# Optimization experiments

Measured on AMD Instinct MI355X. Metric: run time of the kernel, lower is better.

## Reference

```python
import jax, jax.numpy as jnp
import numpy as np

B, QUE, VAL, D = 4, 128, 128, 512

def setup_inputs() -> dict:
    key = jax.random.key(0)
    k = jax.random.split(key, 8)
    return {
        "qs_1": jax.random.normal(k[0], (B, QUE, D), jnp.float32),
        "qs_2": jax.random.normal(k[1], (B, QUE, D), jnp.float32),  # unused by forward, kept for signature fidelity
        "ks":   jax.random.normal(k[2], (B, VAL, D), jnp.float32),
        "vs":   jax.random.normal(k[3], (B, VAL, D), jnp.float32),
        "sg_mask": jax.random.randint(k[4], (B, VAL), 0, 2).astype(bool),  # True = masked
        "W1":  jax.random.normal(k[5], (D, D), jnp.float32) / np.sqrt(D),
        "b1":  jnp.zeros((D,), jnp.float32),
        "Wse": jax.random.normal(k[6], (D, D), jnp.float32) / np.sqrt(D),
        "bse": jnp.zeros((D,), jnp.float32),
        "W2":  jax.random.normal(k[7], (D, 1), jnp.float32) / np.sqrt(D),
        "b2":  jnp.zeros((1,), jnp.float32),
    }

def reference(qs_1, qs_2, ks, vs, sg_mask, W1, b1, Wse, bse, W2, b2):
    # Pairwise query-key elementwise product: [B, que, val, d]
    x = qs_1[:, :, None, :] * ks[:, None, :, :]
    # linear1: Linear(d,d) + ReLU (dropout = identity at eval)
    h = jax.nn.relu(jnp.einsum('bqvd,de->bqve', x, W1) + b1)
    # linear2: Linear(d,1) + ReLU -> scalar score per (q, v) pair
    s = jax.nn.relu(jnp.einsum('bqvd,do->bqvo', h, W2) + b2)[..., 0]  # [B, que, val]
    m = sg_mask[:, None, :]                      # [B, 1, val], True = masked out
    # masked mean of h over the val axis (masked_fill(0) then divide by valid count)
    h = jnp.where(m[..., None], 0.0, h)
    denom = jnp.sum(~sg_mask, axis=-1).astype(h.dtype)      # [B]
    mean = h.sum(axis=2) / denom[:, None, None]             # [B, que, d]
    # squeeze-excitation gate: sigmoid(relu(Linear(d,d)))
    gate = jax.nn.sigmoid(jax.nn.relu(mean @ Wse + bse))    # [B, que, d]
    # masked softmax over val, weighted sum of values
    s = jnp.where(m, -1e9, s)
    w = jax.nn.softmax(s, axis=-1)                          # [B, que, val]
    out = jnp.einsum('bqv,bvd->bqd', w, vs)                 # [B, que, d]
    return gate * out
```

## Files before the change

kernel.cpp:

```cpp
#include <hip/hip_runtime.h>
#include <stdint.h>
#include <stddef.h>

#define BDIM 4
#define QUE  128
#define VAL  128
#define DD   512
#define BQ   (BDIM*QUE)
#define BK   64

typedef float    f32x4 __attribute__((ext_vector_type(4)));
typedef float    f32x2 __attribute__((ext_vector_type(2)));
typedef _Float16 f16x8 __attribute__((ext_vector_type(8)));
typedef _Float16 f16x4 __attribute__((ext_vector_type(4)));
typedef _Float16 f16x2 __attribute__((ext_vector_type(2)));

typedef const __attribute__((address_space(1))) void* gas_ptr;
typedef __attribute__((address_space(3))) void*       las_ptr;

__device__ __forceinline__ void async_copy16(const void* g, void* l) {
    __builtin_amdgcn_global_load_lds((gas_ptr)g, (las_ptr)l, 16, 0, 0);
}

__global__ __launch_bounds__(256) void prep_kernel(const float* __restrict__ W1,
                                                   _Float16* __restrict__ W1T,
                                                   const float* __restrict__ Wse,
                                                   _Float16* __restrict__ WseT,
                                                   const float* __restrict__ vs,
                                                   _Float16* __restrict__ vsT,
                                                   const float* __restrict__ qs1,
                                                   _Float16* __restrict__ qH,
                                                   const float* __restrict__ ks,
                                                   _Float16* __restrict__ ksH) {
    const int gx = blockIdx.x, gy = blockIdx.y;
    if (gy >= 36) {
        const float* src = (gy == 36) ? qs1 : ks;
        _Float16*    dst = (gy == 36) ? qH  : ksH;
        size_t base = (size_t)gx * 16384 + threadIdx.x * 4;
        #pragma unroll 4
        for (int i = 0; i < 16; ++i) {
            f32x4 w = *(const f32x4*)(src + base + (size_t)i * 1024);
            f16x4 h;
            h[0] = (_Float16)w[0]; h[1] = (_Float16)w[1];
            h[2] = (_Float16)w[2]; h[3] = (_Float16)w[3];
            *(f16x4*)(dst + base + (size_t)i * 1024) = h;
        }
        return;
    }
    __shared__ float tile[32][33];
    const int tx = threadIdx.x & 31;
    const int ty = threadIdx.x >> 5;
    if (gy < 32) {
        const float* src = (gy < 16) ? W1  : Wse;
        _Float16*    dst = (gy < 16) ? W1T : WseT;
        int a0 = gx * 32;
        int b0 = (gy & 15) * 32;
        #pragma unroll
        for (int r = 0; r < 4; ++r)
            tile[ty + r*8][tx] = src[(size_t)(a0 + ty + r*8) * DD + b0 + tx];
        __syncthreads();
        #pragma unroll
        for (int r = 0; r < 4; ++r) {
            int el = ty + r*8;
            dst[(size_t)(b0 + el) * DD + a0 + tx] = (_Float16)tile[tx][el];
        }
    } else {
        int bb = gy - 32;
        const float* src = vs  + (size_t)bb * VAL * DD;
        _Float16*    dst = vsT + (size_t)bb * DD * VAL;
        int b0 = gx * 32;
        for (int vt = 0; vt < 4; ++vt) {
            int a0 = vt * 32;
            __syncthreads();
            #pragma unroll
            for (int r = 0; r < 4; ++r)
                tile[ty + r*8][tx] = src[(size_t)(a0 + ty + r*8) * DD + b0 + tx];
            __syncthreads();
            #pragma unroll
            for (int r = 0; r < 4; ++r) {
                int el = ty + r*8;
                dst[(size_t)(b0 + el) * VAL + a0 + tx] = (_Float16)tile[tx][el];
            }
        }
    }
}

__global__ __launch_bounds__(512, 4) void gemm_h_kernel(
    const _Float16* __restrict__ qH,
    const _Float16* __restrict__ ksH,
    const int*   __restrict__ sgmask,
    const _Float16* __restrict__ W1T,
    const float* __restrict__ b1,
    const float* __restrict__ W2,
    float* __restrict__ s_part,
    float* __restrict__ meansum)
{
    __shared__ _Float16 Ah[128 * BK];
    __shared__ _Float16 Bh[256 * BK];
    __shared__ float sred[4][VAL];
    __shared__ float msumLDS[2][256];

    const int tid  = threadIdx.x;
    const int bq   = blockIdx.x;
    const int gy   = blockIdx.y;
    const int b    = bq >> 7;
    const int lane = tid & 63;
    const int wid  = tid >> 6;
    const int wm   = wid >> 2;
    const int wn   = wid & 3;
    const int quad = lane >> 4;
    const int lr   = lane & 15;

    f32x4 acc[4][4];
    #pragma unroll
    for (int i = 0; i < 4; ++i)
        #pragma unroll
        for (int j = 0; j < 4; ++j) acc[i][j] = (f32x4){0.f, 0.f, 0.f, 0.f};

    const int ar0 = tid >> 3;
    const int slt = tid & 7;
    const int ca0 = (slt - (ar0 & 7)) & 7;
    const _Float16* ksrow0 = ksH + ((size_t)b * VAL + ar0)      * DD + ca0 * 8;
    const _Float16* ksrow1 = ksH + ((size_t)b * VAL + 64 + ar0) * DD + ca0 * 8;
    const _Float16* qrow_g = qH  + (size_t)bq * DD + ca0 * 8;
    const int aoff0 = tid * 8;
    const int aoff1 = (512 + tid) * 8;

    const _Float16* gB[4];
    int ldsBoff[4];
    #pragma unroll
    for (int j = 0; j < 4; ++j) {
        int chunk = j * 512 + tid;
        int row   = chunk >> 3;
        int c     = ((chunk & 7) - (row & 7)) & 7;
        gB[j] = W1T + (size_t)(gy * 256 + row) * DD + c * 8;
        ldsBoff[j] = (j * 512 + wid * 64) * 8;
    }

    int faoff[4], fboff[4];
    #pragma unroll
    for (int mt = 0; mt < 4; ++mt) {
        int row = wm * 64 + mt * 16 + lr;
        faoff[mt] = row * BK + (((quad + row) & 7) << 3);
    }
    #pragma unroll
    for (int nt = 0; nt < 4; ++nt) {
        int row = wn * 64 + nt * 16 + lr;
        fboff[nt] = row * BK + (((quad + row) & 7) << 3);
    }

    f16x8 kv0 = *(const f16x8*)(ksrow0);
    f16x8 kv1 = *(const f16x8*)(ksrow1);
    f16x8 qv  = *(const f16x8*)(qrow_g);

    for (int i = 0; i < 8; ++i) {
        const int kk = i * BK;
        #pragma unroll
        for (int j = 0; j < 4; ++j)
            async_copy16(gB[j] + kk, &Bh[ldsBoff[j]]);
        *(f16x8*)&Ah[aoff0] = kv0 * qv;
        *(f16x8*)&Ah[aoff1] = kv1 * qv;
        __syncthreads();

        if (i < 7) {
            kv0 = *(const f16x8*)(ksrow0 + kk + BK);
            kv1 = *(const f16x8*)(ksrow1 + kk + BK);
            qv  = *(const f16x8*)(qrow_g + kk + BK);
        }
        #pragma unroll
        for (int sub = 0; sub < 2; ++sub) {
            const int sx = sub << 5;
            f16x8 fa[4];
            #pragma unroll
            for (int mt = 0; mt < 4; ++mt)
                fa[mt] = *(const f16x8*)&Ah[faoff[mt] ^ sx];
            #pragma unroll
            for (int nt = 0; nt < 4; ++nt) {
                f16x8 fb = *(const f16x8*)&Bh[fboff[nt] ^ sx];
                #pragma unroll
                for (int mt = 0; mt < 4; ++mt)
                    acc[mt][nt] = __builtin_amdgcn_mfma_f32_16x16x32_f16(fa[mt], fb, acc[mt][nt], 0, 0, 0);
            }
        }
        __syncthreads();
    }

    float b1v[4], w2v[4];
    #pragma unroll
    for (int nt = 0; nt < 4; ++nt) {
        int col = gy*256 + wn*64 + nt*16 + lr;
        b1v[nt] = b1[col];
        w2v[nt] = W2[col];
    }
    float msum[4] = {0.f, 0.f, 0.f, 0.f};
    #pragma unroll
    for (int mt = 0; mt < 4; ++mt) {
        #pragma unroll
        for (int reg = 0; reg < 4; ++reg) {
            int v = wm*64 + mt*16 + quad*4 + reg;
            int masked = sgmask[b * VAL + v];
            float sacc = 0.f;
            #pragma unroll
            for (int nt = 0; nt < 4; ++nt) {
                float h = acc[mt][nt][reg] + b1v[nt];
                h = fmaxf(h, 0.f);
                sacc += h * w2v[nt];
                if (!masked) msum[nt] += h;
            }
            sacc += __shfl_xor(sacc, 1);
            sacc += __shfl_xor(sacc, 2);
            sacc += __shfl_xor(sacc, 4);
            sacc += __shfl_xor(sacc, 8);
            if (lr == 0) sred[wn][v] = sacc;
        }
    }
    #pragma unroll
    for (int nt = 0; nt < 4; ++nt) {
        float m = msum[nt];
        m += __shfl_xor(m, 16);
        m += __shfl_xor(m, 32);
        if (lane < 16) msumLDS[wm][wn*64 + nt*16 + lr] = m;
    }
    __syncthreads();
    if (tid < 128) {
        s_part[((size_t)bq * 2 + gy) * VAL + tid] =
            sred[0][tid] + sred[1][tid] + sred[2][tid] + sred[3][tid];
    } else if (tid >= 256) {
        int c = tid - 256;
        meansum[(size_t)bq * DD + gy*256 + c] = msumLDS[0][c] + msumLDS[1][c];
    }
}

#define MPAD 514
#define WPAD 130
__global__ __launch_bounds__(256) void final_kernel(
    const float* __restrict__ s_part,
    const float* __restrict__ msum,
    const int*   __restrict__ sgmask,
    const _Float16* __restrict__ WseT,
    const _Float16* __restrict__ vsT,
    const float* __restrict__ bse,
    const float* __restrict__ b2,
    float* __restrict__ out)
{
    __shared__ _Float16 meanLDS[32 * MPAD];
    __shared__ _Float16 wLDS[32 * WPAD];
    __shared__ _Float16 BLDS[32 * WPAD];

    const int tid  = threadIdx.x;
    const int q0   = blockIdx.x * 32;
    const int d0   = blockIdx.y * 32;
    const int b    = q0 >> 7;
    const int lane = tid & 63;
    const int wid  = tid >> 6;
    const int wm   = wid >> 1, wn = wid & 1;
    const int quad = lane >> 4;
    const int lr   = lane & 15;
    const int r    = tid >> 3;
    const int sl   = tid & 7;

    const float b2v = b2[0];
    const int   bq  = q0 + r;
    const float* sp = s_part + (size_t)bq * 2 * VAL;
    float vals[16];
    int   msk[16];
    float smax = -3.4e38f;
    #pragma unroll
    for (int i4 = 0; i4 < 4; ++i4) {
        f32x4 s0 = *(const f32x4*)(sp + sl*16 + i4*4);
        f32x4 s1 = *(const f32x4*)(sp + VAL + sl*16 + i4*4);
        #pragma unroll
        for (int j = 0; j < 4; ++j) {
            int idx = i4*4 + j;
            int v   = sl*16 + idx;
            float s = fmaxf(s0[j] + s1[j] + b2v, 0.f);
            int m   = sgmask[b * VAL + v];
            msk[idx] = m;
            if (m) s = -1e9f;
            vals[idx] = s;
            smax = fmaxf(smax, s);
        }
    }
    smax = fmaxf(smax, __shfl_xor(smax, 1));
    smax = fmaxf(smax, __shfl_xor(smax, 2));
    smax = fmaxf(smax, __shfl_xor(smax, 4));
    float sume = 0.f, cnt = 0.f;
    #pragma unroll
    for (int i = 0; i < 16; ++i) {
        vals[i] = __expf(vals[i] - smax);
        sume += vals[i];
        cnt  += msk[i] ? 0.f : 1.f;
    }
    sume += __shfl_xor(sume, 1);  cnt += __shfl_xor(cnt, 1);
    sume += __shfl_xor(sume, 2);  cnt += __shfl_xor(cnt, 2);
    sume += __shfl_xor(sume, 4);  cnt += __shfl_xor(cnt, 4);
    const float invse = 1.f / sume;
    const float invd  = 1.f / cnt;
    f16x8 wv0, wv1;
    #pragma unroll
    for (int i = 0; i < 8; ++i) {
        wv0[i] = (_Float16)(vals[i]     * invse);
        wv1[i] = (_Float16)(vals[i + 8] * invse);
    }
    *(f16x8*)&wLDS[r * WPAD + sl*16]     = wv0;
    *(f16x8*)&wLDS[r * WPAD + sl*16 + 8] = wv1;
    const float* mrow = msum + (size_t)bq * DD;
    #pragma unroll
    for (int i = 0; i < 8; ++i) {
        int e = i*64 + sl*8;
        f32x4 m0 = *(const f32x4*)(mrow + e);
        f32x4 m1 = *(const f32x4*)(mrow + e + 4);
        f16x8 mh;
        #pragma unroll
        for (int c = 0; c < 4; ++c) {
            mh[c]     = (_Float16)(m0[c] * invd);
            mh[c + 4] = (_Float16)(m1[c] * invd);
        }
        *(f16x8*)&meanLDS[r * MPAD + e] = mh;
    }
    __syncthreads();

    f32x4 accg = (f32x4){0.f, 0.f, 0.f, 0.f};
    const int a_off = (wm*16 + lr) * MPAD + quad*8;
    const int b_off = (wn*16 + lr) * WPAD + quad*8;
    const int st_off = r * WPAD + sl*16;
    #pragma unroll
    for (int cc = 0; cc < 4; ++cc) {
        const _Float16* wrow = WseT + (size_t)(d0 + r) * DD + cc*128 + sl*16;
        f16x8 bw0 = *(const f16x8*)(wrow);
        f16x8 bw1 = *(const f16x8*)(wrow + 8);
        *(f16x8*)&BLDS[st_off]     = bw0;
        *(f16x8*)&BLDS[st_off + 8] = bw1;
        __syncthreads();
        #pragma unroll
        for (int ks = 0; ks < 4; ++ks) {
            f16x8 fa = *(const f16x8*)&meanLDS[a_off + cc*128 + ks*32];
            f16x8 fb = *(const f16x8*)&BLDS[b_off + ks*32];
            accg = __builtin_amdgcn_mfma_f32_16x16x32_f16(fa, fb, accg, 0, 0, 0);
        }
        __syncthreads();
    }

    {
        const _Float16* vrow = vsT + ((size_t)b * DD + d0 + r) * VAL + sl*16;
        f16x8 bv0 = *(const f16x8*)(vrow);
        f16x8 bv1 = *(const f16x8*)(vrow + 8);
        *(f16x8*)&BLDS[st_off]     = bv0;
        *(f16x8*)&BLDS[st_off + 8] = bv1;
    }
    __syncthreads();
    f32x4 acco = (f32x4){0.f, 0.f, 0.f, 0.f};
    const int w_off = (wm*16 + lr) * WPAD + quad*8;
    #pragma unroll
    for (int ks = 0; ks < 4; ++ks) {
        f16x8 fa = *(const f16x8*)&wLDS[w_off + ks*32];
        f16x8 fb = *(const f16x8*)&BLDS[b_off + ks*32];
        acco = __builtin_amdgcn_mfma_f32_16x16x32_f16(fa, fb, acco, 0, 0, 0);
    }

    const int d = d0 + wn*16 + lr;
    const float bsev = bse[d];
    #pragma unroll
    for (int reg = 0; reg < 4; ++reg) {
        int q = q0 + wm*16 + quad*4 + reg;
        float g = fmaxf(accg[reg] + bsev, 0.f);
        g = 1.f / (1.f + __expf(-g));
        out[(size_t)q * DD + d] = g * acco[reg];
    }
}

extern "C" void kernel_launch(void* const* d_in, const int* in_sizes, int n_in,
                              void* d_out, int out_size, void* d_ws, size_t ws_size,
                              hipStream_t stream) {
    (void)in_sizes; (void)n_in; (void)out_size; (void)ws_size;
    const float* qs1 = (const float*)d_in[0];
    const float* ks  = (const float*)d_in[2];
    const float* vs  = (const float*)d_in[3];
    const int*   sg  = (const int*)d_in[4];
    const float* W1  = (const float*)d_in[5];
    const float* b1  = (const float*)d_in[6];
    const float* Wse = (const float*)d_in[7];
    const float* bse = (const float*)d_in[8];
    const float* W2  = (const float*)d_in[9];
    const float* b2  = (const float*)d_in[10];
    float* out = (float*)d_out;

    char* ws = (char*)d_ws;
    _Float16* W1T    = (_Float16*)(ws);
    _Float16* WseT   = (_Float16*)(ws + (512 << 10));
    _Float16* vsT    = (_Float16*)(ws + (1 << 20));
    float*    s_part = (float*)(ws + (1536 << 10));
    float*    msum   = (float*)(ws + (2 << 20));
    _Float16* qH     = (_Float16*)(ws + (3 << 20));
    _Float16* ksH    = (_Float16*)(ws + (3 << 20) + (512 << 10));

    prep_kernel<<<dim3(16, 38), 256, 0, stream>>>(W1, W1T, Wse, WseT, vs, vsT,
                                                  qs1, qH, ks, ksH);
    gemm_h_kernel<<<dim3(BQ, 2), 512, 0, stream>>>(qH, ksH, sg, W1T, b1, W2, s_part, msum);
    final_kernel<<<dim3(16, 16), 256, 0, stream>>>(s_part, msum, sg, WseT, vsT, bse, b2, out);
}
```

Baseline: 128.4 us.

## Halve gemm_h N-tile to 128 and double-buffer the A tile with register-staged B fragments

The main GEMM now uses 256-thread blocks, each covering 128 output columns, with four column blocks per query row instead of two. The A operand (q*k products) is double-buffered in LDS. The B fragments for the whole K-step are pulled into registers before a barrier, so the next B async copy and the next A product write can overlap the MFMA work on the current buffers. The final kernel and the workspace layout are updated to reduce four partial score slices instead of two. The aim is more blocks in flight and fewer stalls from load-then-sync, at the cost of more register pressure, extra s_part traffic, and each block recomputing the A products.

```diff
diff --git a/kernel.cpp b/kernel.cpp
--- a/kernel.cpp
+++ b/kernel.cpp
@@ -85,7 +85,7 @@
     }
 }
 
-__global__ __launch_bounds__(512, 4) void gemm_h_kernel(
+__global__ __launch_bounds__(256, 3) void gemm_h_kernel(
     const _Float16* __restrict__ qH,
     const _Float16* __restrict__ ksH,
     const int*   __restrict__ sgmask,
@@ -95,10 +95,10 @@
     float* __restrict__ s_part,
     float* __restrict__ meansum)
 {
-    __shared__ _Float16 Ah[128 * BK];
-    __shared__ _Float16 Bh[256 * BK];
-    __shared__ float sred[4][VAL];
-    __shared__ float msumLDS[2][256];
+    __shared__ _Float16 Ah[2][128 * BK];
+    __shared__ _Float16 Bh[128 * BK];
+    __shared__ float sred[2][VAL];
+    __shared__ float msumLDS[2][128];
 
     const int tid  = threadIdx.x;
     const int bq   = blockIdx.x;
@@ -106,8 +106,8 @@
     const int b    = bq >> 7;
     const int lane = tid & 63;
     const int wid  = tid >> 6;
-    const int wm   = wid >> 2;
-    const int wn   = wid & 3;
+    const int wm   = wid >> 1;
+    const int wn   = wid & 1;
     const int quad = lane >> 4;
     const int lr   = lane & 15;
 
@@ -120,22 +120,13 @@
     const int ar0 = tid >> 3;
     const int slt = tid & 7;
     const int ca0 = (slt - (ar0 & 7)) & 7;
-    const _Float16* ksrow0 = ksH + ((size_t)b * VAL + ar0)      * DD + ca0 * 8;
-    const _Float16* ksrow1 = ksH + ((size_t)b * VAL + 64 + ar0) * DD + ca0 * 8;
+    const _Float16* ksrow0 = ksH + ((size_t)b * VAL + ar0) * DD + ca0 * 8;
     const _Float16* qrow_g = qH  + (size_t)bq * DD + ca0 * 8;
     const int aoff0 = tid * 8;
-    const int aoff1 = (512 + tid) * 8;
-
-    const _Float16* gB[4];
-    int ldsBoff[4];
-    #pragma unroll
-    for (int j = 0; j < 4; ++j) {
-        int chunk = j * 512 + tid;
-        int row   = chunk >> 3;
-        int c     = ((chunk & 7) - (row & 7)) & 7;
-        gB[j] = W1T + (size_t)(gy * 256 + row) * DD + c * 8;
-        ldsBoff[j] = (j * 512 + wid * 64) * 8;
-    }
+
+    const int brow0 = tid >> 3;
+    const int bc0   = ((tid & 7) - (brow0 & 7)) & 7;
+    const _Float16* gB0 = W1T + (size_t)(gy * 128 + brow0) * DD + bc0 * 8;
 
     int faoff[4], fboff[4];
     #pragma unroll
@@ -149,46 +140,76 @@
         fboff[nt] = row * BK + (((quad + row) & 7) << 3);
     }
 
-    f16x8 kv0 = *(const f16x8*)(ksrow0);
-    f16x8 kv1 = *(const f16x8*)(ksrow1);
-    f16x8 qv  = *(const f16x8*)(qrow_g);
-
+    #pragma unroll
+    for (int j = 0; j < 4; ++j)
+        async_copy16(gB0 + (size_t)j * 32 * DD, &Bh[(j * 256 + wid * 64) * 8]);
+    f16x8 kv[4], qv;
+    #pragma unroll
+    for (int j = 0; j < 4; ++j)
+        kv[j] = *(const f16x8*)(ksrow0 + (size_t)j * 32 * DD);
+    qv = *(const f16x8*)(qrow_g);
+    #pragma unroll
+    for (int j = 0; j < 4; ++j)
+        *(f16x8*)&Ah[0][aoff0 + j * 2048] = kv[j] * qv;
+    #pragma unroll
+    for (int j = 0; j < 4; ++j)
+        kv[j] = *(const f16x8*)(ksrow0 + (size_t)j * 32 * DD + BK);
+    qv = *(const f16x8*)(qrow_g + BK);
+    __syncthreads();
+
+    int p = 0;
     for (int i = 0; i < 8; ++i) {
-        const int kk = i * BK;
-        #pragma unroll
-        for (int j = 0; j < 4; ++j)
-            async_copy16(gB[j] + kk, &Bh[ldsBoff[j]]);
-        *(f16x8*)&Ah[aoff0] = kv0 * qv;
-        *(f16x8*)&Ah[aoff1] = kv1 * qv;
-        __syncthreads();
+        f16x8 fbr[2][4];
+        #pragma unroll
+        for (int s = 0; s < 2; ++s) {
+            const int sx = s << 5;
+            #pragma unroll
+            for (int nt = 0; nt < 4; ++nt)
+                fbr[s][nt] = *(const f16x8*)&Bh[fboff[nt] ^ sx];
+        }
+        asm volatile("s_waitcnt lgkmcnt(0)" ::: "memory");
+        __builtin_amdgcn_s_barrier();
 
         if (i < 7) {
-            kv0 = *(const f16x8*)(ksrow0 + kk + BK);
-            kv1 = *(const f16x8*)(ksrow1 + kk + BK);
-            qv  = *(const f16x8*)(qrow_g + kk + BK);
-        }
-        #pragma unroll
-        for (int sub = 0; sub < 2; ++sub) {
-            const int sx = sub << 5;
+            const int kk = (i + 1) * BK;
+            #pragma unroll
+            for (int j = 0; j < 4; ++j)
+                *(f16x8*)&Ah[p ^ 1][aoff0 + j * 2048] = kv[j] * qv;
+            if (i < 6) {
+                #pragma unroll
+                for (int j = 0; j < 4; ++j)
+                    kv[j] = *(const f16x8*)(ksrow0 + (size_t)j * 32 * DD + kk + BK);
+                qv = *(const f16x8*)(qrow_g + kk + BK);
+            }
+            #pragma unroll
+            for (int j = 0; j < 4; ++j)
+                async_copy16(gB0 + (size_t)j * 32 * DD + kk,
+                             &Bh[(j * 256 + wid * 64) * 8]);
+        }
+
+        const _Float16* Ab = &Ah[p][0];
+        #pragma unroll
+        for (int s = 0; s < 2; ++s) {
+            const int sx = s << 5;
             f16x8 fa[4];
             #pragma unroll
             for (int mt = 0; mt < 4; ++mt)
-                fa[mt] = *(const f16x8*)&Ah[faoff[mt] ^ sx];
-            #pragma unroll
-            for (int nt = 0; nt < 4; ++nt) {
-                f16x8 fb = *(const f16x8*)&Bh[fboff[nt] ^ sx];
+                fa[mt] = *(const f16x8*)&Ab[faoff[mt] ^ sx];
+            #pragma unroll
+            for (int nt = 0; nt < 4; ++nt)
                 #pragma unroll
                 for (int mt = 0; mt < 4; ++mt)
-                    acc[mt][nt] = __builtin_amdgcn_mfma_f32_16x16x32_f16(fa[mt], fb, acc[mt][nt], 0, 0, 0);
-            }
+                    acc[mt][nt] = __builtin_amdgcn_mfma_f32_16x16x32_f16(
+                        fa[mt], fbr[s][nt], acc[mt][nt], 0, 0, 0);
         }
         __syncthreads();
+        p ^= 1;
     }
 
     float b1v[4], w2v[4];
     #pragma unroll
     for (int nt = 0; nt < 4; ++nt) {
-        int col = gy*256 + wn*64 + nt*16 + lr;
+        int col = gy*128 + wn*64 + nt*16 + lr;
         b1v[nt] = b1[col];
         w2v[nt] = W2[col];
     }
@@ -223,11 +244,10 @@
     }
     __syncthreads();
     if (tid < 128) {
-        s_part[((size_t)bq * 2 + gy) * VAL + tid] =
-            sred[0][tid] + sred[1][tid] + sred[2][tid] + sred[3][tid];
-    } else if (tid >= 256) {
-        int c = tid - 256;
-        meansum[(size_t)bq * DD + gy*256 + c] = msumLDS[0][c] + msumLDS[1][c];
+        s_part[((size_t)bq * 4 + gy) * VAL + tid] = sred[0][tid] + sred[1][tid];
+    } else {
+        int c = tid - 128;
+        meansum[(size_t)bq * DD + gy*128 + c] = msumLDS[0][c] + msumLDS[1][c];
     }
 }
 
@@ -261,19 +281,21 @@
 
     const float b2v = b2[0];
     const int   bq  = q0 + r;
-    const float* sp = s_part + (size_t)bq * 2 * VAL;
+    const float* sp = s_part + (size_t)bq * 4 * VAL;
     float vals[16];
     int   msk[16];
     float smax = -3.4e38f;
     #pragma unroll
     for (int i4 = 0; i4 < 4; ++i4) {
-        f32x4 s0 = *(const f32x4*)(sp + sl*16 + i4*4);
-        f32x4 s1 = *(const f32x4*)(sp + VAL + sl*16 + i4*4);
+        f32x4 s0 = *(const f32x4*)(sp +           sl*16 + i4*4);
+        f32x4 s1 = *(const f32x4*)(sp + VAL     + sl*16 + i4*4);
+        f32x4 s2 = *(const f32x4*)(sp + 2*VAL   + sl*16 + i4*4);
+        f32x4 s3 = *(const f32x4*)(sp + 3*VAL   + sl*16 + i4*4);
         #pragma unroll
         for (int j = 0; j < 4; ++j) {
             int idx = i4*4 + j;
             int v   = sl*16 + idx;
-            float s = fmaxf(s0[j] + s1[j] + b2v, 0.f);
+            float s = fmaxf(s0[j] + s1[j] + s2[j] + s3[j] + b2v, 0.f);
             int m   = sgmask[b * VAL + v];
             msk[idx] = m;
             if (m) s = -1e9f;
@@ -390,12 +412,12 @@
     _Float16* WseT   = (_Float16*)(ws + (512 << 10));
     _Float16* vsT    = (_Float16*)(ws + (1 << 20));
     float*    s_part = (float*)(ws + (1536 << 10));
-    float*    msum   = (float*)(ws + (2 << 20));
-    _Float16* qH     = (_Float16*)(ws + (3 << 20));
-    _Float16* ksH    = (_Float16*)(ws + (3 << 20) + (512 << 10));
+    float*    msum   = (float*)(ws + (2560 << 10));
+    _Float16* qH     = (_Float16*)(ws + (3584 << 10));
+    _Float16* ksH    = (_Float16*)(ws + (4096 << 10));
 
     prep_kernel<<<dim3(16, 38), 256, 0, stream>>>(W1, W1T, Wse, WseT, vs, vsT,
                                                   qs1, qH, ks, ksH);
-    gemm_h_kernel<<<dim3(BQ, 2), 512, 0, stream>>>(qH, ksH, sg, W1T, b1, W2, s_part, msum);
+    gemm_h_kernel<<<dim3(BQ, 4), 256, 0, stream>>>(qH, ksH, sg, W1T, b1, W2, s_part, msum);
     final_kernel<<<dim3(16, 16), 256, 0, stream>>>(s_part, msum, sg, WseT, vsT, bse, b2, out);
 }
```

Measured after the change: 130.4 us. About the same (+1.6%).

## Fuse three kernels into one persistent kernel with grid-wide atomic barriers

Applied to the files above, without the earlier changes.

Merges the prep, main GEMM and final kernels into a single 512-block launch that separates its phases with atomic-counter grid barriers. This removes two kernel launch gaps and their inter-kernel drain. In exchange, each block runs the old gy=0/1 column halves one after the other, so there are half as many concurrent GEMM blocks. The design also depends on all 512 blocks being co-resident, otherwise the barrier deadlocks, and it adds a memset launch to reset the counter.

```diff
diff --git a/kernel.cpp b/kernel.cpp
--- a/kernel.cpp
+++ b/kernel.cpp
@@ -8,12 +8,11 @@
 #define DD   512
 #define BQ   (BDIM*QUE)
 #define BK   64
+#define GRID 512
 
 typedef float    f32x4 __attribute__((ext_vector_type(4)));
-typedef float    f32x2 __attribute__((ext_vector_type(2)));
 typedef _Float16 f16x8 __attribute__((ext_vector_type(8)));
 typedef _Float16 f16x4 __attribute__((ext_vector_type(4)));
-typedef _Float16 f16x2 __attribute__((ext_vector_type(2)));
 
 typedef const __attribute__((address_space(1))) void* gas_ptr;
 typedef __attribute__((address_space(3))) void*       las_ptr;
@@ -22,350 +21,373 @@
     __builtin_amdgcn_global_load_lds((gas_ptr)g, (las_ptr)l, 16, 0, 0);
 }
 
-__global__ __launch_bounds__(256) void prep_kernel(const float* __restrict__ W1,
-                                                   _Float16* __restrict__ W1T,
-                                                   const float* __restrict__ Wse,
-                                                   _Float16* __restrict__ WseT,
-                                                   const float* __restrict__ vs,
-                                                   _Float16* __restrict__ vsT,
-                                                   const float* __restrict__ qs1,
-                                                   _Float16* __restrict__ qH,
-                                                   const float* __restrict__ ks,
-                                                   _Float16* __restrict__ ksH) {
-    const int gx = blockIdx.x, gy = blockIdx.y;
-    if (gy >= 36) {
-        const float* src = (gy == 36) ? qs1 : ks;
-        _Float16*    dst = (gy == 36) ? qH  : ksH;
-        size_t base = (size_t)gx * 16384 + threadIdx.x * 4;
-        #pragma unroll 4
-        for (int i = 0; i < 16; ++i) {
-            f32x4 w = *(const f32x4*)(src + base + (size_t)i * 1024);
-            f16x4 h;
-            h[0] = (_Float16)w[0]; h[1] = (_Float16)w[1];
-            h[2] = (_Float16)w[2]; h[3] = (_Float16)w[3];
-            *(f16x4*)(dst + base + (size_t)i * 1024) = h;
-        }
-        return;
+__device__ __forceinline__ void gsync(unsigned* ctr) {
+    __syncthreads();
+    if (threadIdx.x == 0) {
+        __threadfence();
+        atomicAdd(ctr, 1u);
+        while (__hip_atomic_load(ctr, __ATOMIC_RELAXED, __HIP_MEMORY_SCOPE_AGENT)
+               < (unsigned)GRID)
+            __builtin_amdgcn_s_sleep(2);
     }
-    __shared__ float tile[32][33];
-    const int tx = threadIdx.x & 31;
-    const int ty = threadIdx.x >> 5;
-    if (gy < 32) {
-        const float* src = (gy < 16) ? W1  : Wse;
-        _Float16*    dst = (gy < 16) ? W1T : WseT;
-        int a0 = gx * 32;
-        int b0 = (gy & 15) * 32;
+    __syncthreads();
+    __threadfence();
+}
+
+#define MPAD 514
+#define WPAD 130
+
+__global__ __launch_bounds__(512, 4) void mega_kernel(
+    const float* __restrict__ qs1, const float* __restrict__ ks,
+    const float* __restrict__ vs,  const int*   __restrict__ sgmask,
+    const float* __restrict__ W1,  const float* __restrict__ b1,
+    const float* __restrict__ Wse, const float* __restrict__ bse,
+    const float* __restrict__ W2,  const float* __restrict__ b2,
+    float* __restrict__ out,
+    _Float16* __restrict__ W1T, _Float16* __restrict__ WseT,
+    _Float16* __restrict__ vsT, float* __restrict__ s_part,
+    float* __restrict__ msum,   _Float16* __restrict__ qH,
+    _Float16* __restrict__ ksH, unsigned* __restrict__ bar)
+{
+    __shared__ char lds[53248] __attribute__((aligned(16)));
+    const int tid = threadIdx.x;
+    const int blk = blockIdx.x;
+
+    if (blk < 256) {
+        const int half = tid >> 8;
+        const int t    = tid & 255;
+        const float* src = half ? Wse : W1;
+        _Float16*    dst = half ? WseT : W1T;
+        float (*tl)[33] = (float(*)[33])(lds + half * 4224);
+        const int a0 = (blk & 15) * 32;
+        const int b0 = (blk >> 4) * 32;
+        const int tx = t & 31, ty = t >> 5;
         #pragma unroll
         for (int r = 0; r < 4; ++r)
-            tile[ty + r*8][tx] = src[(size_t)(a0 + ty + r*8) * DD + b0 + tx];
+            tl[ty + r*8][tx] = src[(size_t)(a0 + ty + r*8) * DD + b0 + tx];
         __syncthreads();
         #pragma unroll
         for (int r = 0; r < 4; ++r) {
             int el = ty + r*8;
-            dst[(size_t)(b0 + el) * DD + a0 + tx] = (_Float16)tile[tx][el];
+            dst[(size_t)(b0 + el) * DD + a0 + tx] = (_Float16)tl[tx][el];
         }
     } else {
-        int bb = gy - 32;
-        const float* src = vs  + (size_t)bb * VAL * DD;
-        _Float16*    dst = vsT + (size_t)bb * DD * VAL;
-        int b0 = gx * 32;
-        for (int vt = 0; vt < 4; ++vt) {
-            int a0 = vt * 32;
-            __syncthreads();
+        const int job = blk - 256;
+        float (*tl)[33] = (float(*)[33])lds;
+        const int bb = job >> 6;
+        const int gx = (job >> 2) & 15;
+        const int vt = job & 3;
+        const float* srcv = vs  + (size_t)bb * VAL * DD;
+        _Float16*    dstv = vsT + (size_t)bb * DD * VAL;
+        const int b0 = gx * 32, a0 = vt * 32;
+        const int tx = tid & 31, ty = (tid >> 5) & 7;
+        if (tid < 256) {
             #pragma unroll
             for (int r = 0; r < 4; ++r)
-                tile[ty + r*8][tx] = src[(size_t)(a0 + ty + r*8) * DD + b0 + tx];
-            __syncthreads();
+                tl[ty + r*8][tx] = srcv[(size_t)(a0 + ty + r*8) * DD + b0 + tx];
+        } else {
+            int idx = job * 256 + (tid - 256);
+            f32x4 w = *(const f32x4*)(qs1 + (size_t)idx * 4);
+            f16x4 h; h[0]=(_Float16)w[0]; h[1]=(_Float16)w[1];
+            h[2]=(_Float16)w[2]; h[3]=(_Float16)w[3];
+            *(f16x4*)(qH + (size_t)idx * 4) = h;
+        }
+        __syncthreads();
+        if (tid < 256) {
             #pragma unroll
             for (int r = 0; r < 4; ++r) {
                 int el = ty + r*8;
-                dst[(size_t)(b0 + el) * VAL + a0 + tx] = (_Float16)tile[tx][el];
-            }
+                dstv[(size_t)(b0 + el) * VAL + a0 + tx] = (_Float16)tl[tx][el];
+            }
+        } else {
+            int idx = job * 256 + (tid - 256);
+            f32x4 w = *(const f32x4*)(ks + (size_t)idx * 4);
+            f16x4 h; h[0]=(_Float16)w[0]; h[1]=(_Float16)w[1];
+            h[2]=(_Float16)w[2]; h[3]=(_Float16)w[3];
+            *(f16x4*)(ksH + (size_t)idx * 4) = h;
         }
     }
-}
-
-__global__ __launch_bounds__(512, 4) void gemm_h_kernel(
-    const _Float16* __restrict__ qH,
-    const _Float16* __restrict__ ksH,
-    const int*   __restrict__ sgmask,
-    const _Float16* __restrict__ W1T,
-    const float* __restrict__ b1,
-    const float* __restrict__ W2,
-    float* __restrict__ s_part,
-    float* __restrict__ meansum)
-{
-    __shared__ _Float16 Ah[128 * BK];
-    __shared__ _Float16 Bh[256 * BK];
-    __shared__ float sred[4][VAL];
-    __shared__ float msumLDS[2][256];
-
-    const int tid  = threadIdx.x;
-    const int bq   = blockIdx.x;
-    const int gy   = blockIdx.y;
-    const int b    = bq >> 7;
-    const int lane = tid & 63;
-    const int wid  = tid >> 6;
-    const int wm   = wid >> 2;
-    const int wn   = wid & 3;
-    const int quad = lane >> 4;
-    const int lr   = lane & 15;
-
-    f32x4 acc[4][4];
-    #pragma unroll
-    for (int i = 0; i < 4; ++i)
+
+    gsync(bar + 0);
+
+    {
+        _Float16* Ah = (_Float16*)lds;
+        _Float16* Bh = (_Float16*)(lds + 16384);
+        float (*sred)[VAL]    = (float(*)[VAL])(lds + 49152);
+        float (*msumLDS)[256] = (float(*)[256])(lds + 51200);
+
+        const int bq   = blk;
+        const int b    = bq >> 7;
+        const int lane = tid & 63;
+        const int wid  = tid >> 6;
+        const int wm   = wid >> 2;
+        const int wn   = wid & 3;
+        const int quad = lane >> 4;
+        const int lr   = lane & 15;
+
+        const int ar0 = tid >> 3;
+        const int slt = tid & 7;
+        const int ca0 = (slt - (ar0 & 7)) & 7;
+        const _Float16* ksrow0 = ksH + ((size_t)b * VAL + ar0)      * DD + ca0 * 8;
+        const _Float16* ksrow1 = ksH + ((size_t)b * VAL + 64 + ar0) * DD + ca0 * 8;
+        const _Float16* qrow_g = qH  + (size_t)bq * DD + ca0 * 8;
+        const int aoff0 = tid * 8;
+        const int aoff1 = (512 + tid) * 8;
+
+        int faoff[4], fboff[4];
         #pragma unroll
-        for (int j = 0; j < 4; ++j) acc[i][j] = (f32x4){0.f, 0.f, 0.f, 0.f};
-
-    const int ar0 = tid >> 3;
-    const int slt = tid & 7;
-    const int ca0 = (slt - (ar0 & 7)) & 7;
-    const _Float16* ksrow0 = ksH + ((size_t)b * VAL + ar0)      * DD + ca0 * 8;
-    const _Float16* ksrow1 = ksH + ((size_t)b * VAL + 64 + ar0) * DD + ca0 * 8;
-    const _Float16* qrow_g = qH  + (size_t)bq * DD + ca0 * 8;
-    const int aoff0 = tid * 8;
-    const int aoff1 = (512 + tid) * 8;
-
-    const _Float16* gB[4];
-    int ldsBoff[4];
-    #pragma unroll
-    for (int j = 0; j < 4; ++j) {
-        int chunk = j * 512 + tid;
-        int row   = chunk >> 3;
-        int c     = ((chunk & 7) - (row & 7)) & 7;
-        gB[j] = W1T + (size_t)(gy * 256 + row) * DD + c * 8;
-        ldsBoff[j] = (j * 512 + wid * 64) * 8;
+        for (int mt = 0; mt < 4; ++mt) {
+            int row = wm * 64 + mt * 16 + lr;
+            faoff[mt] = row * BK + (((quad + row) & 7) << 3);
+        }
+        #pragma unroll
+        for (int nt = 0; nt < 4; ++nt) {
+            int row = wn * 64 + nt * 16 + lr;
+            fboff[nt] = row * BK + (((quad + row) & 7) << 3);
+        }
+
+        for (int gy = 0; gy < 2; ++gy) {
+            __syncthreads();
+
+            const _Float16* gB[4];
+            int ldsBoff[4];
+            #pragma unroll
+            for (int j = 0; j < 4; ++j) {
+                int chunk = j * 512 + tid;
+                int row   = chunk >> 3;
+                int c     = ((chunk & 7) - (row & 7)) & 7;
+                gB[j] = W1T + (size_t)(gy * 256 + row) * DD + c * 8;
+                ldsBoff[j] = (j * 512 + wid * 64) * 8;
+            }
+
+            f32x4 acc[4][4];
+            #pragma unroll
+            for (int i = 0; i < 4; ++i)
+                #pragma unroll
+                for (int j = 0; j < 4; ++j) acc[i][j] = (f32x4){0.f,0.f,0.f,0.f};
+
+            f16x8 kv0 = *(const f16x8*)(ksrow0);
+            f16x8 kv1 = *(const f16x8*)(ksrow1);
+            f16x8 qv  = *(const f16x8*)(qrow_g);
+
+            for (int i = 0; i < 8; ++i) {
+                const int kk = i * BK;
+                #pragma unroll
+                for (int j = 0; j < 4; ++j)
+                    async_copy16(gB[j] + kk, &Bh[ldsBoff[j]]);
+                *(f16x8*)&Ah[aoff0] = kv0 * qv;
+                *(f16x8*)&Ah[aoff1] = kv1 * qv;
+                __syncthreads();
+
+                if (i < 7) {
+                    kv0 = *(const f16x8*)(ksrow0 + kk + BK);
+                    kv1 = *(const f16x8*)(ksrow1 + kk + BK);
+                    qv  = *(const f16x8*)(qrow_g + kk + BK);
+                }
+                #pragma unroll
+                for (int s = 0; s < 2; ++s) {
+                    const int sx = s << 5;
+                    f16x8 fa[4];
+                    #pragma unroll
+                    for (int mt = 0; mt < 4; ++mt)
+                        fa[mt] = *(const f16x8*)&Ah[faoff[mt] ^ sx];
+                    #pragma unroll
+                    for (int nt = 0; nt < 4; ++nt) {
+                        f16x8 fb = *(const f16x8*)&Bh[fboff[nt] ^ sx];
+                        #pragma unroll
+                        for (int mt = 0; mt < 4; ++mt)
+                            acc[mt][nt] = __builtin_amdgcn_mfma_f32_16x16x32_f16(
+                                fa[mt], fb, acc[mt][nt], 0, 0, 0);
+                    }
+                }
+                __syncthreads();
+            }
+
+            float b1v[4], w2v[4];
+            #pragma unroll
+            for (int nt = 0; nt < 4; ++nt) {
+                int col = gy*256 + wn*64 + nt*16 + lr;
+                b1v[nt] = b1[col];
+                w2v[nt] = W2[col];
+            }
+            float msm[4] = {0.f, 0.f, 0.f, 0.f};
+            #pragma unroll
+            for (int mt = 0; mt < 4; ++mt) {
+                #pragma unroll
+                for (int reg = 0; reg < 4; ++reg) {
+                    int v = wm*64 + mt*16 + quad*4 + reg;
+                    int masked = sgmask[b * VAL + v];
+                    float sacc = 0.f;
+                    #pragma unroll
+                    for (int nt = 0; nt < 4; ++nt) {
+                        float h = acc[mt][nt][reg] + b1v[nt];
+                        h = fmaxf(h, 0.f);
+                        sacc += h * w2v[nt];
+                        if (!masked) msm[nt] += h;
+                    }
+                    sacc += __shfl_xor(sacc, 1);
+                    sacc += __shfl_xor(sacc, 2);
+                    sacc += __shfl_xor(sacc, 4);
+                    sacc += __shfl_xor(sacc, 8);
+                    if (lr == 0) sred[wn][v] = sacc;
+                }
+            }
+            #pragma unroll
+            for (int nt = 0; nt < 4; ++nt) {
+                float m = msm[nt];
+                m += __shfl_xor(m, 16);
+                m += __shfl_xor(m, 32);
+                if (lane < 16) msumLDS[wm][wn*64 + nt*16 + lr] = m;
+            }
+            __syncthreads();
+            if (tid < 128) {
+                s_part[((size_t)bq * 2 + gy) * VAL + tid] =
+                    sred[0][tid] + sred[1][tid] + sred[2][tid] + sred[3][tid];
+            } else if (tid >= 256 && tid < 384) {
+                int c = tid - 256;
+                msum[(size_t)bq * DD + gy*256 + c]       = msumLDS[0][c] + msumLDS[1][c];
+            } else if (tid >= 384) {
+                int c = tid - 384 + 128;
+                msum[(size_t)bq * DD + gy*256 + c]       = msumLDS[0][c] + msumLDS[1][c];
+            }
+        }
     }
 
-    int faoff[4], fboff[4];
-    #pragma unroll
-    for (int mt = 0; mt < 4; ++mt) {
-        int row = wm * 64 + mt * 16 + lr;
-        faoff[mt] = row * BK + (((quad + row) & 7) << 3);
-    }
-    #pragma unroll
-    for (int nt = 0; nt < 4; ++nt) {
-        int row = wn * 64 + nt * 16 + lr;
-        fboff[nt] = row * BK + (((quad + row) & 7) << 3);
-    }
-
-    f16x8 kv0 = *(const f16x8*)(ksrow0);
-    f16x8 kv1 = *(const f16x8*)(ksrow1);
-    f16x8 qv  = *(const f16x8*)(qrow_g);
-
-    for (int i = 0; i < 8; ++i) {
-        const int kk = i * BK;
+    gsync(bar + 1);
+
+    if (blk < 256) {
+        _Float16* meanLDS = (_Float16*)lds;
+        _Float16* wLDS    = (_Float16*)(lds + 32896);
+        _Float16* BLDS    = (_Float16*)(lds + 41216);
+
+        const bool act = tid < 256;
+        const int q0   = (blk >> 4) * 32;
+        const int d0   = (blk & 15) * 32;
+        const int b    = q0 >> 7;
+        const int lane = tid & 63;
+        const int wid  = tid >> 6;
+        const int wm   = wid >> 1, wn = wid & 1;
+        const int quad = lane >> 4;
+        const int lr   = lane & 15;
+        const int r    = (tid >> 3) & 31;
+        const int sl   = tid & 7;
+
+        const int a_off  = (wm*16 + lr) * MPAD + quad*8;
+        const int b_off  = (wn*16 + lr) * WPAD + quad*8;
+        const int st_off = r * WPAD + sl*16;
+
+        if (act) {
+            const float b2v = b2[0];
+            const int   bq  = q0 + r;
+            const float* sp = s_part + (size_t)bq * 2 * VAL;
+            float vals[16];
+            int   msk[16];
+            float smax = -3.4e38f;
+            #pragma unroll
+            for (int i4 = 0; i4 < 4; ++i4) {
+                f32x4 s0 = *(const f32x4*)(sp + sl*16 + i4*4);
+                f32x4 s1 = *(const f32x4*)(sp + VAL + sl*16 + i4*4);
+                #pragma unroll
+                for (int j = 0; j < 4; ++j) {
+                    int idx = i4*4 + j;
+                    int v   = sl*16 + idx;
+                    float s = fmaxf(s0[j] + s1[j] + b2v, 0.f);
+                    int m   = sgmask[b * VAL + v];
+                    msk[idx] = m;
+                    if (m) s = -1e9f;
+                    vals[idx] = s;
+                    smax = fmaxf(smax, s);
+                }
+            }
+            smax = fmaxf(smax, __shfl_xor(smax, 1));
+            smax = fmaxf(smax, __shfl_xor(smax, 2));
+            smax = fmaxf(smax, __shfl_xor(smax, 4));
+            float sume = 0.f, cnt = 0.f;
+            #pragma unroll
+            for (int i = 0; i < 16; ++i) {
+                vals[i] = __expf(vals[i] - smax);
+                sume += vals[i];
+                cnt  += msk[i] ? 0.f : 1.f;
+            }
+            sume += __shfl_xor(sume, 1);  cnt += __shfl_xor(cnt, 1);
+            sume += __shfl_xor(sume, 2);  cnt += __shfl_xor(cnt, 2);
+            sume += __shfl_xor(sume, 4);  cnt += __shfl_xor(cnt, 4);
+            const float invse = 1.f / sume;
+            const float invd  = 1.f / cnt;
+            f16x8 wv0, wv1;
+            #pragma unroll
+            for (int i = 0; i < 8; ++i) {
+                wv0[i] = (_Float16)(vals[i]     * invse);
+                wv1[i] = (_Float16)(vals[i + 8] * invse);
+            }
+            *(f16x8*)&wLDS[r * WPAD + sl*16]     = wv0;
+            *(f16x8*)&wLDS[r * WPAD + sl*16 + 8] = wv1;
+            const float* mrow = msum + (size_t)bq * DD;
+            #pragma unroll
+            for (int i = 0; i < 8; ++i) {
+                int e = i*64 + sl*8;
+                f32x4 m0 = *(const f32x4*)(mrow + e);
+                f32x4 m1 = *(const f32x4*)(mrow + e + 4);
+                f16x8 mh;
+                #pragma unroll
+                for (int c = 0; c < 4; ++c) {
+                    mh[c]     = (_Float16)(m0[c] * invd);
+                    mh[c + 4] = (_Float16)(m1[c] * invd);
+                }
+                *(f16x8*)&meanLDS[r * MPAD + e] = mh;
+            }
+        }
+        __syncthreads();
+
+        f32x4 accg = (f32x4){0.f, 0.f, 0.f, 0.f};
         #pragma unroll
-        for (int j = 0; j < 4; ++j)
-            async_copy16(gB[j] + kk, &Bh[ldsBoff[j]]);
-        *(f16x8*)&Ah[aoff0] = kv0 * qv;
-        *(f16x8*)&Ah[aoff1] = kv1 * qv;
+        for (int cc = 0; cc < 4; ++cc) {
+            if (act) {
+                const _Float16* wrow = WseT + (size_t)(d0 + r) * DD + cc*128 + sl*16;
+                f16x8 bw0 = *(const f16x8*)(wrow);
+                f16x8 bw1 = *(const f16x8*)(wrow + 8);
+                *(f16x8*)&BLDS[st_off]     = bw0;
+                *(f16x8*)&BLDS[st_off + 8] = bw1;
+            }
+            __syncthreads();
+            if (act) {
+                #pragma unroll
+                for (int ksi = 0; ksi < 4; ++ksi) {
+                    f16x8 fa = *(const f16x8*)&meanLDS[a_off + cc*128 + ksi*32];
+                    f16x8 fb = *(const f16x8*)&BLDS[b_off + ksi*32];
+                    accg = __builtin_amdgcn_mfma_f32_16x16x32_f16(fa, fb, accg, 0, 0, 0);
+                }
+            }
+            __syncthreads();
+        }
+
+        if (act) {
+            const _Float16* vrow = vsT + ((size_t)b * DD + d0 + r) * VAL + sl*16;
+            f16x8 bv0 = *(const f16x8*)(vrow);
+            f16x8 bv1 = *(const f16x8*)(vrow + 8);
+            *(f16x8*)&BLDS[st_off]     = bv0;
+            *(f16x8*)&BLDS[st_off + 8] = bv1;
+        }
         __syncthreads();
-
-        if (i < 7) {
-            kv0 = *(const f16x8*)(ksrow0 + kk + BK);
-            kv1 = *(const f16x8*)(ksrow1 + kk + BK);
-            qv  = *(const f16x8*)(qrow_g + kk + BK);
-        }
-        #pragma unroll
-        for (int sub = 0; sub < 2; ++sub) {
-            const int sx = sub << 5;
-            f16x8 fa[4];
-            #pragma unroll
-            for (int mt = 0; mt < 4; ++mt)
-                fa[mt] = *(const f16x8*)&Ah[faoff[mt] ^ sx];
-            #pragma unroll
-            for (int nt = 0; nt < 4; ++nt) {
-                f16x8 fb = *(const f16x8*)&Bh[fboff[nt] ^ sx];
-                #pragma unroll
-                for (int mt = 0; mt < 4; ++mt)
-                    acc[mt][nt] = __builtin_amdgcn_mfma_f32_16x16x32_f16(fa[mt], fb, acc[mt][nt], 0, 0, 0);
-            }
-        }
-        __syncthreads();
-    }
-
-    float b1v[4], w2v[4];
-    #pragma unroll
-    for (int nt = 0; nt < 4; ++nt) {
-        int col = gy*256 + wn*64 + nt*16 + lr;
-        b1v[nt] = b1[col];
-        w2v[nt] = W2[col];
-    }
-    float msum[4] = {0.f, 0.f, 0.f, 0.f};
-    #pragma unroll
-    for (int mt = 0; mt < 4; ++mt) {
-        #pragma unroll
-        for (int reg = 0; reg < 4; ++reg) {
-            int v = wm*64 + mt*16 + quad*4 + reg;
-            int masked = sgmask[b * VAL + v];
-            float sacc = 0.f;
-            #pragma unroll
-            for (int nt = 0; nt < 4; ++nt) {
-                float h = acc[mt][nt][reg] + b1v[nt];
-                h = fmaxf(h, 0.f);
-                sacc += h * w2v[nt];
-                if (!masked) msum[nt] += h;
-            }
-            sacc += __shfl_xor(sacc, 1);
-            sacc += __shfl_xor(sacc, 2);
-            sacc += __shfl_xor(sacc, 4);
-            sacc += __shfl_xor(sacc, 8);
-            if (lr == 0) sred[wn][v] = sacc;
-        }
-    }
-    #pragma unroll
-    for (int nt = 0; nt < 4; ++nt) {
-        float m = msum[nt];
-        m += __shfl_xor(m, 16);
-        m += __shfl_xor(m, 32);
-        if (lane < 16) msumLDS[wm][wn*64 + nt*16 + lr] = m;
-    }
-    __syncthreads();
-    if (tid < 128) {
-        s_part[((size_t)bq * 2 + gy) * VAL + tid] =
-            sred[0][tid] + sred[1][tid] + sred[2][tid] + sred[3][tid];
-    } else if (tid >= 256) {
-        int c = tid - 256;
-        meansum[(size_t)bq * DD + gy*256 + c] = msumLDS[0][c] + msumLDS[1][c];
-    }
-}
-
-#define MPAD 514
-#define WPAD 130
-__global__ __launch_bounds__(256) void final_kernel(
-    const float* __restrict__ s_part,
-    const float* __restrict__ msum,
-    const int*   __restrict__ sgmask,
-    const _Float16* __restrict__ WseT,
-    const _Float16* __restrict__ vsT,
-    const float* __restrict__ bse,
-    const float* __restrict__ b2,
-    float* __restrict__ out)
-{
-    __shared__ _Float16 meanLDS[32 * MPAD];
-    __shared__ _Float16 wLDS[32 * WPAD];
-    __shared__ _Float16 BLDS[32 * WPAD];
-
-    const int tid  = threadIdx.x;
-    const int q0   = blockIdx.x * 32;
-    const int d0   = blockIdx.y * 32;
-    const int b    = q0 >> 7;
-    const int lane = tid & 63;
-    const int wid  = tid >> 6;
-    const int wm   = wid >> 1, wn = wid & 1;
-    const int quad = lane >> 4;
-    const int lr   = lane & 15;
-    const int r    = tid >> 3;
-    const int sl   = tid & 7;
-
-    const float b2v = b2[0];
-    const int   bq  = q0 + r;
-    const float* sp = s_part + (size_t)bq * 2 * VAL;
-    float vals[16];
-    int   msk[16];
-    float smax = -3.4e38f;
-    #pragma unroll
-    for (int i4 = 0; i4 < 4; ++i4) {
-        f32x4 s0 = *(const f32x4*)(sp + sl*16 + i4*4);
-        f32x4 s1 = *(const f32x4*)(sp + VAL + sl*16 + i4*4);
-        #pragma unroll
-        for (int j = 0; j < 4; ++j) {
-            int idx = i4*4 + j;
-            int v   = sl*16 + idx;
-            float s = fmaxf(s0[j] + s1[j] + b2v, 0.f);
-            int m   = sgmask[b * VAL + v];
-            msk[idx] = m;
-            if (m) s = -1e9f;
-            vals[idx] = s;
-            smax = fmaxf(smax, s);
-        }
-    }
-    smax = fmaxf(smax, __shfl_xor(smax, 1));
-    smax = fmaxf(smax, __shfl_xor(smax, 2));
-    smax = fmaxf(smax, __shfl_xor(smax, 4));
-    float sume = 0.f, cnt = 0.f;
-    #pragma unroll
-    for (int i = 0; i < 16; ++i) {
-        vals[i] = __expf(vals[i] - smax);
-        sume += vals[i];
-        cnt  += msk[i] ? 0.f : 1.f;
-    }
-    sume += __shfl_xor(sume, 1);  cnt += __shfl_xor(cnt, 1);
-    sume += __shfl_xor(sume, 2);  cnt += __shfl_xor(cnt, 2);
-    sume += __shfl_xor(sume, 4);  cnt += __shfl_xor(cnt, 4);
-    const float invse = 1.f / sume;
-    const float invd  = 1.f / cnt;
-    f16x8 wv0, wv1;
-    #pragma unroll
-    for (int i = 0; i < 8; ++i) {
-        wv0[i] = (_Float16)(vals[i]     * invse);
-        wv1[i] = (_Float16)(vals[i + 8] * invse);
-    }
-    *(f16x8*)&wLDS[r * WPAD + sl*16]     = wv0;
-    *(f16x8*)&wLDS[r * WPAD + sl*16 + 8] = wv1;
-    const float* mrow = msum + (size_t)bq * DD;
-    #pragma unroll
-    for (int i = 0; i < 8; ++i) {
-        int e = i*64 + sl*8;
-        f32x4 m0 = *(const f32x4*)(mrow + e);
-        f32x4 m1 = *(const f32x4*)(mrow + e + 4);
-        f16x8 mh;
-        #pragma unroll
-        for (int c = 0; c < 4; ++c) {
-            mh[c]     = (_Float16)(m0[c] * invd);
-            mh[c + 4] = (_Float16)(m1[c] * invd);
-        }
-        *(f16x8*)&meanLDS[r * MPAD + e] = mh;
-    }
-    __syncthreads();
-
-    f32x4 accg = (f32x4){0.f, 0.f, 0.f, 0.f};
-    const int a_off = (wm*16 + lr) * MPAD + quad*8;
-    const int b_off = (wn*16 + lr) * WPAD + quad*8;
-    const int st_off = r * WPAD + sl*16;
-    #pragma unroll
-    for (int cc = 0; cc < 4; ++cc) {
-        const _Float16* wrow = WseT + (size_t)(d0 + r) * DD + cc*128 + sl*16;
-        f16x8 bw0 = *(const f16x8*)(wrow);
-        f16x8 bw1 = *(const f16x8*)(wrow + 8);
-        *(f16x8*)&BLDS[st_off]     = bw0;
-        *(f16x8*)&BLDS[st_off + 8] = bw1;
-        __syncthreads();
-        #pragma unroll
-        for (int ks = 0; ks < 4; ++ks) {
-            f16x8 fa = *(const f16x8*)&meanLDS[a_off + cc*128 + ks*32];
-            f16x8 fb = *(const f16x8*)&BLDS[b_off + ks*32];
-            accg = __builtin_amdgcn_mfma_f32_16x16x32_f16(fa, fb, accg, 0, 0, 0);
-        }
-        __syncthreads();
-    }
-
-    {
-        const _Float16* vrow = vsT + ((size_t)b * DD + d0 + r) * VAL + sl*16;
-        f16x8 bv0 = *(const f16x8*)(vrow);
-        f16x8 bv1 = *(const f16x8*)(vrow + 8);
-        *(f16x8*)&BLDS[st_off]     = bv0;
-        *(f16x8*)&BLDS[st_off + 8] = bv1;
-    }
-    __syncthreads();
-    f32x4 acco = (f32x4){0.f, 0.f, 0.f, 0.f};
-    const int w_off = (wm*16 + lr) * WPAD + quad*8;
-    #pragma unroll
-    for (int ks = 0; ks < 4; ++ks) {
-        f16x8 fa = *(const f16x8*)&wLDS[w_off + ks*32];
-        f16x8 fb = *(const f16x8*)&BLDS[b_off + ks*32];
-        acco = __builtin_amdgcn_mfma_f32_16x16x32_f16(fa, fb, acco, 0, 0, 0);
-    }
-
-    const int d = d0 + wn*16 + lr;
-    const float bsev = bse[d];
-    #pragma unroll
-    for (int reg = 0; reg < 4; ++reg) {
-        int q = q0 + wm*16 + quad*4 + reg;
-        float g = fmaxf(accg[reg] + bsev, 0.f);
-        g = 1.f / (1.f + __expf(-g));
-        out[(size_t)q * DD + d] = g * acco[reg];
+        if (act) {
+            f32x4 acco = (f32x4){0.f, 0.f, 0.f, 0.f};
+            const int w_off = (wm*16 + lr) * WPAD + quad*8;
+            #pragma unroll
+            for (int ksi = 0; ksi < 4; ++ksi) {
+                f16x8 fa = *(const f16x8*)&wLDS[w_off + ksi*32];
+                f16x8 fb = *(const f16x8*)&BLDS[b_off + ksi*32];
+                acco = __builtin_amdgcn_mfma_f32_16x16x32_f16(fa, fb, acco, 0, 0, 0);
+            }
+            const int d = d0 + wn*16 + lr;
+            const float bsev = bse[d];
+            #pragma unroll
+            for (int reg = 0; reg < 4; ++reg) {
+                int q = q0 + wm*16 + quad*4 + reg;
+                float g = fmaxf(accg[reg] + bsev, 0.f);
+                g = 1.f / (1.f + __expf(-g));
+                out[(size_t)q * DD + d] = g * acco[reg];
+            }
+        }
     }
 }
 
@@ -393,9 +415,10 @@
     float*    msum   = (float*)(ws + (2 << 20));
     _Float16* qH     = (_Float16*)(ws + (3 << 20));
     _Float16* ksH    = (_Float16*)(ws + (3 << 20) + (512 << 10));
-
-    prep_kernel<<<dim3(16, 38), 256, 0, stream>>>(W1, W1T, Wse, WseT, vs, vsT,
-                                                  qs1, qH, ks, ksH);
-    gemm_h_kernel<<<dim3(BQ, 2), 512, 0, stream>>>(qH, ksH, sg, W1T, b1, W2, s_part, msum);
-    final_kernel<<<dim3(16, 16), 256, 0, stream>>>(s_part, msum, sg, WseT, vsT, bse, b2, out);
+    unsigned* bar    = (unsigned*)(ws + (4 << 20));
+
+    hipMemsetAsync(bar, 0, 256, stream);
+    mega_kernel<<<dim3(GRID), dim3(512), 0, stream>>>(
+        qs1, ks, vs, sg, W1, b1, Wse, bse, W2, b2, out,
+        W1T, WseT, vsT, s_part, msum, qH, ksH, bar);
 }
```

After: 322.5 us. +151.2%, slower.
